# Kernel tuning notes

Measured on AMD Instinct MI355X. Metric: run time of the kernel, lower is better.

The kernel has to match this reference:

```python
import jax, jax.numpy as jnp
import numpy as np

N = 8192
F_IN = 512
F_OUT = 64
BETA = 0.5      # conf.beta
ALPHA = 0.2     # LeakyReLU negative slope
NEG_INF = -9e15


def setup_inputs() -> dict:
    key = jax.random.key(0)
    k1, k2, k3, k4, k5 = jax.random.split(key, 5)
    h = jax.random.normal(k1, (N, F_IN), dtype=jnp.float32)
    adj = jax.random.randint(k2, (N, N), 0, 2, dtype=jnp.int32)
    M = jax.random.uniform(k3, (N, N), dtype=jnp.float32)
    W = jax.random.normal(k4, (F_IN, F_OUT), dtype=jnp.float32) * (1.414 / np.sqrt(F_IN))
    a = jax.random.normal(k5, (2 * F_OUT, 1), dtype=jnp.float32) * 0.1
    return {"h": h, "adj": adj, "M": M, "W": W, "a": a}


def reference(h, adj, M, W, a):
    Wh = h @ W                                   # [N, F_OUT]
    adjf = adj.astype(Wh.dtype)
    H = BETA * M + (1.0 - BETA) * adjf           # [N, N] mixed adjacency
    # additive GAT score: e_ij = leakyrelu(a1.Wh_i + a2.(H Wh)_j)
    Wh1 = Wh @ a[:F_OUT]                         # [N, 1]
    Wh2 = (H @ Wh) @ a[F_OUT:]                   # [N, 1]
    e = jax.nn.leaky_relu(Wh1 + Wh2.T, negative_slope=ALPHA)  # [N, N]
    att = jnp.where(adj > 0, e, NEG_INF)
    att = jax.nn.softmax(att, axis=1)            # masked row softmax
    # dropout omitted (eval mode, training=False)
    h_prime = att @ Wh                           # [N, F_OUT]
    return jax.nn.elu(h_prime)                   # concat=True path
```

## Files before the change

### kernel.cpp

```cpp
#include <hip/hip_runtime.h>

#define NN 8192
#define FIN 512
#define FO 64

typedef __attribute__((ext_vector_type(8))) short short8;
typedef __attribute__((ext_vector_type(16))) float f32x16;
typedef __attribute__((ext_vector_type(4))) unsigned int uintx4;
typedef __attribute__((ext_vector_type(4))) int intv4;
typedef __attribute__((ext_vector_type(4))) float fltv4;
typedef unsigned short u16;
typedef unsigned int u32;
typedef unsigned long long u64;

__device__ inline u16 f2bf(float x) {
  u32 u = __builtin_bit_cast(u32, x);
  return (u16)((u + 0x7FFFu + ((u >> 16) & 1u)) >> 16);
}

__device__ inline u32 bfpack2(float a, float b, float& sum) {
  u32 ua = __builtin_bit_cast(u32, a);
  u32 ub = __builtin_bit_cast(u32, b);
  ua += 0x7FFFu + ((ua >> 16) & 1u);
  ub += 0x7FFFu + ((ub >> 16) & 1u);
  sum += __builtin_bit_cast(float, ua & 0xFFFF0000u);
  sum += __builtin_bit_cast(float, ub & 0xFFFF0000u);
  return (ua >> 16) | (ub & 0xFFFF0000u);
}

__global__ __launch_bounds__(256) void k1_wh(const float* __restrict__ h,
    const float* __restrict__ W, const float* __restrict__ a,
    float* __restrict__ s, float* __restrict__ v, u16* __restrict__ whb) {
  int tid = threadIdx.x;
  int row = blockIdx.x * 16 + (tid >> 4);
  int fq = (tid & 15) << 2;
  const float* hr = h + (size_t)row * FIN;
  float ax = 0.f, ay = 0.f, az = 0.f, aw = 0.f;
  #pragma unroll 4
  for (int k = 0; k < FIN; k += 4) {
    float4 h4 = *(const float4*)(hr + k);
    float4 w0 = *(const float4*)(W + (size_t)(k + 0) * FO + fq);
    float4 w1 = *(const float4*)(W + (size_t)(k + 1) * FO + fq);
    float4 w2 = *(const float4*)(W + (size_t)(k + 2) * FO + fq);
    float4 w3 = *(const float4*)(W + (size_t)(k + 3) * FO + fq);
    ax += h4.x * w0.x + h4.y * w1.x + h4.z * w2.x + h4.w * w3.x;
    ay += h4.x * w0.y + h4.y * w1.y + h4.z * w2.y + h4.w * w3.y;
    az += h4.x * w0.z + h4.y * w1.z + h4.z * w2.z + h4.w * w3.z;
    aw += h4.x * w0.w + h4.y * w1.w + h4.z * w2.w + h4.w * w3.w;
  }
  ushort4 st4;
  st4.x = f2bf(ax); st4.y = f2bf(ay); st4.z = f2bf(az); st4.w = f2bf(aw);
  *(ushort4*)(whb + (size_t)row * FO + fq) = st4;
  float4 a1 = *(const float4*)(a + fq);
  float4 a2 = *(const float4*)(a + FO + fq);
  float sp = ax * a1.x + ay * a1.y + az * a1.z + aw * a1.w;
  float vp = ax * a2.x + ay * a2.y + az * a2.z + aw * a2.w;
  #pragma unroll
  for (int d = 1; d < 16; d <<= 1) { sp += __shfl_xor(sp, d); vp += __shfl_xor(vp, d); }
  if ((tid & 15) == 0) { s[row] = sp; v[row] = vp; }
}

__global__ __launch_bounds__(256) void k1b_pack(const u16* __restrict__ whb,
                                               u16* __restrict__ bpack) {
  __shared__ __attribute__((aligned(16))) u16 ld[64 * 64];
  int tid = threadIdx.x;
  const uint4* src = (const uint4*)(whb + (size_t)blockIdx.x * 64 * 64);
  uint4* dst = (uint4*)ld;
  dst[tid] = src[tid];
  dst[tid + 256] = src[tid + 256];
  __syncthreads();
  int lane = tid & 63;
  int w = tid >> 6;
  int ks = blockIdx.x * 4 + w;
  int m = lane & 31;
  int half = lane >> 5;
  #pragma unroll
  for (int tt = 0; tt < 2; ++tt) {
    u32 o0, o1, o2, o3;
    int krow = w * 16 + half * 8;
    int n = tt * 32 + m;
    o0 = (u32)ld[(krow + 0) * 64 + n] | ((u32)ld[(krow + 1) * 64 + n] << 16);
    o1 = (u32)ld[(krow + 2) * 64 + n] | ((u32)ld[(krow + 3) * 64 + n] << 16);
    o2 = (u32)ld[(krow + 4) * 64 + n] | ((u32)ld[(krow + 5) * 64 + n] << 16);
    o3 = (u32)ld[(krow + 6) * 64 + n] | ((u32)ld[(krow + 7) * 64 + n] << 16);
    uint4 ov; ov.x = o0; ov.y = o1; ov.z = o2; ov.w = o3;
    *(uint4*)(bpack + (((size_t)ks * 2 + tt) * 64 + lane) * 8) = ov;
  }
}

__global__ __launch_bounds__(256) void k2_hv(const int* __restrict__ adj,
    const float* __restrict__ M, const float* __restrict__ v,
    float* __restrict__ t, u64* __restrict__ bm) {
  int i = blockIdx.x;
  int tid = threadIdx.x;
  int lane = tid & 63;
  int w = tid >> 6;
  const intv4* arow = (const intv4*)(adj + (size_t)i * NN);
  const fltv4* mrow = (const fltv4*)(M + (size_t)i * NN);
  const fltv4* v4 = (const fltv4*)v;
  float acc = 0.f;
  #pragma unroll
  for (int it = 0; it < 8; ++it) {
    int idx = it * 256 + tid;
    intv4 a4 = __builtin_nontemporal_load(arow + idx);
    fltv4 m4 = __builtin_nontemporal_load(mrow + idx);
    fltv4 vv = v4[idx];
    acc += m4.x * vv.x + m4.y * vv.y + m4.z * vv.z + m4.w * vv.w;
    acc += (a4.x ? vv.x : 0.f) + (a4.y ? vv.y : 0.f) + (a4.z ? vv.z : 0.f) + (a4.w ? vv.w : 0.f);
    u64 b0 = __ballot(a4.x != 0);
    u64 b1 = __ballot(a4.y != 0);
    u64 b2 = __ballot(a4.z != 0);
    u64 b3 = __ballot(a4.w != 0);
    if (lane == 0) {
      size_t base = (size_t)i * 128 + it * 16 + w * 4;
      bm[base + 0] = b0; bm[base + 1] = b1; bm[base + 2] = b2; bm[base + 3] = b3;
    }
  }
  #pragma unroll
  for (int d = 1; d < 64; d <<= 1) acc += __shfl_xor(acc, d);
  __shared__ float red[4];
  if (lane == 0) red[w] = acc;
  __syncthreads();
  if (tid == 0) t[i] = 0.5f * (red[0] + red[1] + red[2] + red[3]);
}

__device__ inline void stage_tile(const u16* __restrict__ bpack, u16* dstbase,
                                  int jt, int w, int lane) {
  const char* g0 = (const char*)bpack + (size_t)jt * 32768 + (size_t)lane * 16;
  #pragma unroll
  for (int cc = 0; cc < 8; ++cc) {
    int chunk = w * 8 + cc;
    const void* gp = g0 + chunk * 1024;
    void* lp = (char*)dstbase + chunk * 1024;
    __builtin_amdgcn_global_load_lds((const __attribute__((address_space(1))) u32*)gp,
                                     (__attribute__((address_space(3))) u32*)lp, 16, 0, 0);
  }
}

__global__ __launch_bounds__(256) void k3_att(const u16* __restrict__ bpack,
    const u64* __restrict__ bm, const float* __restrict__ t,
    const float* __restrict__ s, float* __restrict__ out) {
  __shared__ __attribute__((aligned(16))) u16 bbuf[2][16384];
  __shared__ __attribute__((aligned(16))) float accbuf[4 * 2 * 64 * 16];
  __shared__ float zbuf[4][64];
  __shared__ float wred[4];
  int tid = threadIdx.x;
  int lane = tid & 63;
  int w = tid >> 6;
  int m = lane & 31;
  int half = lane >> 5;
  int i0 = blockIdx.x << 5;
  int row = i0 + m;
  float srow = s[row];
  stage_tile(bpack, bbuf[0], 0, w, lane);
  float lmax = -3e38f;
  const float4* t4 = (const float4*)t;
  #pragma unroll
  for (int r = 0; r < 8; ++r) {
    float4 tv = t4[r * 256 + tid];
    lmax = fmaxf(fmaxf(lmax, fmaxf(tv.x, tv.y)), fmaxf(tv.z, tv.w));
  }
  #pragma unroll
  for (int d = 1; d < 64; d <<= 1) lmax = fmaxf(lmax, __shfl_xor(lmax, d));
  if (lane == 0) wred[w] = lmax;
  __syncthreads();
  float tmax = fmaxf(fmaxf(wred[0], wred[1]), fmaxf(wred[2], wred[3]));
  float um = srow + tmax;
  float mxv = fmaxf(um, 0.2f * um);

  f32x16 acc0, acc1;
  #pragma unroll
  for (int r = 0; r < 16; ++r) { acc0[r] = 0.f; acc1[r] = 0.f; }
  float zpart = 0.f;
  int cur = 0;
  for (int jt = 0; jt < 32; ++jt) {
    __syncthreads();
    if (jt + 1 < 32) stage_tile(bpack, bbuf[cur ^ 1], jt + 1, w, lane);
    const u64* wp = bm + (size_t)row * 128 + ((jt >> 2) << 4) + ((jt & 3) << 2);
    u64 wd0 = wp[0], wd1 = wp[1], wd2 = wp[2], wd3 = wp[3];
    const float* tb = t + (jt << 8) + (w << 6) + (half << 3);
    #pragma unroll
    for (int c = 0; c < 4; ++c) {
      int ks = (w << 2) + c;
      float4 t0 = *(const float4*)(tb + (c << 4));
      float4 t1 = *(const float4*)(tb + (c << 4) + 4);
      int sh = (w << 4) + (c << 2) + (half << 1);
      u32 q0 = (u32)(wd0 >> sh), q1 = (u32)(wd1 >> sh);
      u32 q2 = (u32)(wd2 >> sh), q3 = (u32)(wd3 >> sh);
      float u0 = srow + t0.x, u1 = srow + t0.y, u2 = srow + t0.z, u3 = srow + t0.w;
      float u4 = srow + t1.x, u5 = srow + t1.y, u6 = srow + t1.z, u7 = srow + t1.w;
      float g0 = __expf(fmaxf(u0, 0.2f * u0) - mxv);
      float g1 = __expf(fmaxf(u1, 0.2f * u1) - mxv);
      float g2 = __expf(fmaxf(u2, 0.2f * u2) - mxv);
      float g3 = __expf(fmaxf(u3, 0.2f * u3) - mxv);
      float g4 = __expf(fmaxf(u4, 0.2f * u4) - mxv);
      float g5 = __expf(fmaxf(u5, 0.2f * u5) - mxv);
      float g6 = __expf(fmaxf(u6, 0.2f * u6) - mxv);
      float g7 = __expf(fmaxf(u7, 0.2f * u7) - mxv);
      float w0 = (q0 & 1u) ? g0 : 0.f;
      float w1 = (q1 & 1u) ? g1 : 0.f;
      float w2 = (q2 & 1u) ? g2 : 0.f;
      float w3 = (q3 & 1u) ? g3 : 0.f;
      float w4 = (q0 & 2u) ? g4 : 0.f;
      float w5 = (q1 & 2u) ? g5 : 0.f;
      float w6 = (q2 & 2u) ? g6 : 0.f;
      float w7 = (q3 & 2u) ? g7 : 0.f;
      uintx4 awv;
      awv.x = bfpack2(w0, w1, zpart);
      awv.y = bfpack2(w2, w3, zpart);
      awv.z = bfpack2(w4, w5, zpart);
      awv.w = bfpack2(w6, w7, zpart);
      short8 af = __builtin_bit_cast(short8, awv);
      short8 b0 = *(const short8*)(bbuf[cur] + (((ks << 1) + 0) * 64 + lane) * 8);
      short8 b1 = *(const short8*)(bbuf[cur] + (((ks << 1) + 1) * 64 + lane) * 8);
      acc0 = __builtin_amdgcn_mfma_f32_32x32x16_bf16(af, b0, acc0, 0, 0, 0);
      acc1 = __builtin_amdgcn_mfma_f32_32x32x16_bf16(af, b1, acc1, 0, 0, 0);
    }
    cur ^= 1;
  }
  __syncthreads();
  zbuf[w][lane] = zpart;
  {
    float* ab = accbuf + (((w << 1) + 0) * 64 + lane) * 16;
    #pragma unroll
    for (int r = 0; r < 16; ++r) ab[r] = acc0[r];
    ab = accbuf + (((w << 1) + 1) * 64 + lane) * 16;
    #pragma unroll
    for (int r = 0; r < 16; ++r) ab[r] = acc1[r];
  }
  __syncthreads();
  int mm = tid >> 3;
  int fb = (tid & 7) << 3;
  float zr = 0.f;
  #pragma unroll
  for (int ww = 0; ww < 4; ++ww) zr += zbuf[ww][mm] + zbuf[ww][mm + 32];
  float inv = 1.f / zr;
  int reg = (mm & 3) + ((mm >> 3) << 2);
  int h2 = (mm >> 2) & 1;
  #pragma unroll
  for (int ff = 0; ff < 8; ++ff) {
    int f = fb + ff;
    int tt = f >> 5;
    int col = f & 31;
    float val = 0.f;
    #pragma unroll
    for (int ww = 0; ww < 4; ++ww)
      val += accbuf[(((ww << 1) + tt) * 64 + col + (h2 << 5)) * 16 + reg];
    float o = val * inv;
    out[((size_t)(i0 + mm) << 6) + f] = o > 0.f ? o : (__expf(o) - 1.f);
  }
}

extern "C" void kernel_launch(void* const* d_in, const int* in_sizes, int n_in,
                              void* d_out, int out_size, void* d_ws, size_t ws_size,
                              hipStream_t stream) {
  const float* h   = (const float*)d_in[0];
  const int*   adj = (const int*)d_in[1];
  const float* M   = (const float*)d_in[2];
  const float* W   = (const float*)d_in[3];
  const float* a   = (const float*)d_in[4];
  float* out = (float*)d_out;
  char* ws = (char*)d_ws;
  u64*  bm    = (u64*)ws;
  u16*  whb   = (u16*)(ws + (8u << 20));
  u16*  bpack = (u16*)(ws + (9u << 20));
  float* s    = (float*)(ws + (10u << 20));
  float* v    = (float*)(ws + (10u << 20) + 32768);
  float* t    = (float*)(ws + (10u << 20) + 65536);

  k1_wh  <<<512, 256, 0, stream>>>(h, W, a, s, v, whb);
  k1b_pack<<<128, 256, 0, stream>>>(whb, bpack);
  k2_hv  <<<NN, 256, 0, stream>>>(adj, M, v, t, bm);
  k3_att <<<256, 256, 0, stream>>>(bpack, bm, t, s, out);
}
```

Measured before the change: 598.2 us.

## Factor softmax exponentials into per-column tables and hoist the global max

The exponent exp(leakyrelu(s_i+t_j)-mx) is split into per-row constants times per-column factors exp(t_j-tmax) or exp(0.2(t_j-tmax)), chosen by the sign of s_i+t_j. A new single-block kernel computes tmax and the two column tables once, which removes per-element exp calls and the per-block max reduction from the attention kernel. In exchange it adds an extra launch and two more global loads per element, and the product form may overflow or underflow differently from the original.

```diff
diff --git a/kernel.cpp b/kernel.cpp
--- a/kernel.cpp
+++ b/kernel.cpp
@@ -124,6 +124,38 @@
   if (tid == 0) t[i] = 0.5f * (red[0] + red[1] + red[2] + red[3]);
 }
 
+__global__ __launch_bounds__(1024) void k2b_prep(const float* __restrict__ t,
+    float* __restrict__ f1, float* __restrict__ f2, float* __restrict__ tmaxg) {
+  __shared__ float red[16];
+  int tid = threadIdx.x;
+  const fltv4* t4 = (const fltv4*)t;
+  fltv4 a = t4[tid];
+  fltv4 b = t4[tid + 1024];
+  float lm = fmaxf(fmaxf(fmaxf(a.x, a.y), fmaxf(a.z, a.w)),
+                   fmaxf(fmaxf(b.x, b.y), fmaxf(b.z, b.w)));
+  #pragma unroll
+  for (int d = 1; d < 64; d <<= 1) lm = fmaxf(lm, __shfl_xor(lm, d));
+  if ((tid & 63) == 0) red[tid >> 6] = lm;
+  __syncthreads();
+  float tmax = red[0];
+  #pragma unroll
+  for (int r = 1; r < 16; ++r) tmax = fmaxf(tmax, red[r]);
+  if (tid == 0) tmaxg[0] = tmax;
+  fltv4 o;
+  o.x = __expf(a.x - tmax); o.y = __expf(a.y - tmax);
+  o.z = __expf(a.z - tmax); o.w = __expf(a.w - tmax);
+  ((fltv4*)f1)[tid] = o;
+  o.x = __expf(b.x - tmax); o.y = __expf(b.y - tmax);
+  o.z = __expf(b.z - tmax); o.w = __expf(b.w - tmax);
+  ((fltv4*)f1)[tid + 1024] = o;
+  o.x = __expf(0.2f * (a.x - tmax)); o.y = __expf(0.2f * (a.y - tmax));
+  o.z = __expf(0.2f * (a.z - tmax)); o.w = __expf(0.2f * (a.w - tmax));
+  ((fltv4*)f2)[tid] = o;
+  o.x = __expf(0.2f * (b.x - tmax)); o.y = __expf(0.2f * (b.y - tmax));
+  o.z = __expf(0.2f * (b.z - tmax)); o.w = __expf(0.2f * (b.w - tmax));
+  ((fltv4*)f2)[tid + 1024] = o;
+}
+
 __device__ inline void stage_tile(const u16* __restrict__ bpack, u16* dstbase,
                                   int jt, int w, int lane) {
   const char* g0 = (const char*)bpack + (size_t)jt * 32768 + (size_t)lane * 16;
@@ -139,11 +171,12 @@
 
 __global__ __launch_bounds__(256) void k3_att(const u16* __restrict__ bpack,
     const u64* __restrict__ bm, const float* __restrict__ t,
-    const float* __restrict__ s, float* __restrict__ out) {
+    const float* __restrict__ f1, const float* __restrict__ f2,
+    const float* __restrict__ s, const float* __restrict__ tmaxg,
+    float* __restrict__ out) {
   __shared__ __attribute__((aligned(16))) u16 bbuf[2][16384];
   __shared__ __attribute__((aligned(16))) float accbuf[4 * 2 * 64 * 16];
   __shared__ float zbuf[4][64];
-  __shared__ float wred[4];
   int tid = threadIdx.x;
   int lane = tid & 63;
   int w = tid >> 6;
@@ -151,22 +184,14 @@
   int half = lane >> 5;
   int i0 = blockIdx.x << 5;
   int row = i0 + m;
+  stage_tile(bpack, bbuf[0], 0, w, lane);
   float srow = s[row];
-  stage_tile(bpack, bbuf[0], 0, w, lane);
-  float lmax = -3e38f;
-  const float4* t4 = (const float4*)t;
-  #pragma unroll
-  for (int r = 0; r < 8; ++r) {
-    float4 tv = t4[r * 256 + tid];
-    lmax = fmaxf(fmaxf(lmax, fmaxf(tv.x, tv.y)), fmaxf(tv.z, tv.w));
-  }
-  #pragma unroll
-  for (int d = 1; d < 64; d <<= 1) lmax = fmaxf(lmax, __shfl_xor(lmax, d));
-  if (lane == 0) wred[w] = lmax;
-  __syncthreads();
-  float tmax = fmaxf(fmaxf(wred[0], wred[1]), fmaxf(wred[2], wred[3]));
+  float tmax = tmaxg[0];
   float um = srow + tmax;
   float mxv = fmaxf(um, 0.2f * um);
+  float E1 = __expf(um - mxv);
+  float E2 = __expf(0.2f * um - mxv);
+  float negs = -srow;
 
   f32x16 acc0, acc1;
   #pragma unroll
@@ -178,25 +203,30 @@
     if (jt + 1 < 32) stage_tile(bpack, bbuf[cur ^ 1], jt + 1, w, lane);
     const u64* wp = bm + (size_t)row * 128 + ((jt >> 2) << 4) + ((jt & 3) << 2);
     u64 wd0 = wp[0], wd1 = wp[1], wd2 = wp[2], wd3 = wp[3];
-    const float* tb = t + (jt << 8) + (w << 6) + (half << 3);
+    int off = (jt << 8) + (w << 6) + (half << 3);
+    const float* tb = t + off;
+    const float* p1 = f1 + off;
+    const float* p2 = f2 + off;
     #pragma unroll
     for (int c = 0; c < 4; ++c) {
       int ks = (w << 2) + c;
       float4 t0 = *(const float4*)(tb + (c << 4));
       float4 t1 = *(const float4*)(tb + (c << 4) + 4);
+      float4 A0 = *(const float4*)(p1 + (c << 4));
+      float4 A1 = *(const float4*)(p1 + (c << 4) + 4);
+      float4 B0 = *(const float4*)(p2 + (c << 4));
+      float4 B1 = *(const float4*)(p2 + (c << 4) + 4);
       int sh = (w << 4) + (c << 2) + (half << 1);
       u32 q0 = (u32)(wd0 >> sh), q1 = (u32)(wd1 >> sh);
       u32 q2 = (u32)(wd2 >> sh), q3 = (u32)(wd3 >> sh);
-      float u0 = srow + t0.x, u1 = srow + t0.y, u2 = srow + t0.z, u3 = srow + t0.w;
-      float u4 = srow + t1.x, u5 = srow + t1.y, u6 = srow + t1.z, u7 = srow + t1.w;
-      float g0 = __expf(fmaxf(u0, 0.2f * u0) - mxv);
-      float g1 = __expf(fmaxf(u1, 0.2f * u1) - mxv);
-      float g2 = __expf(fmaxf(u2, 0.2f * u2) - mxv);
-      float g3 = __expf(fmaxf(u3, 0.2f * u3) - mxv);
-      float g4 = __expf(fmaxf(u4, 0.2f * u4) - mxv);
-      float g5 = __expf(fmaxf(u5, 0.2f * u5) - mxv);
-      float g6 = __expf(fmaxf(u6, 0.2f * u6) - mxv);
-      float g7 = __expf(fmaxf(u7, 0.2f * u7) - mxv);
+      float g0 = (t0.x >= negs) ? E1 * A0.x : E2 * B0.x;
+      float g1 = (t0.y >= negs) ? E1 * A0.y : E2 * B0.y;
+      float g2 = (t0.z >= negs) ? E1 * A0.z : E2 * B0.z;
+      float g3 = (t0.w >= negs) ? E1 * A0.w : E2 * B0.w;
+      float g4 = (t1.x >= negs) ? E1 * A1.x : E2 * B1.x;
+      float g5 = (t1.y >= negs) ? E1 * A1.y : E2 * B1.y;
+      float g6 = (t1.z >= negs) ? E1 * A1.z : E2 * B1.z;
+      float g7 = (t1.w >= negs) ? E1 * A1.w : E2 * B1.w;
       float w0 = (q0 & 1u) ? g0 : 0.f;
       float w1 = (q1 & 1u) ? g1 : 0.f;
       float w2 = (q2 & 1u) ? g2 : 0.f;
@@ -267,9 +297,13 @@
   float* s    = (float*)(ws + (10u << 20));
   float* v    = (float*)(ws + (10u << 20) + 32768);
   float* t    = (float*)(ws + (10u << 20) + 65536);
-
-  k1_wh  <<<512, 256, 0, stream>>>(h, W, a, s, v, whb);
+  float* f1   = (float*)(ws + (10u << 20) + 98304);
+  float* f2   = (float*)(ws + (10u << 20) + 131072);
+  float* tmx  = (float*)(ws + (10u << 20) + 163840);
+
+  k1_wh   <<<512, 256, 0, stream>>>(h, W, a, s, v, whb);
   k1b_pack<<<128, 256, 0, stream>>>(whb, bpack);
-  k2_hv  <<<NN, 256, 0, stream>>>(adj, M, v, t, bm);
-  k3_att <<<256, 256, 0, stream>>>(bpack, bm, t, s, out);
-}
+  k2_hv   <<<NN, 256, 0, stream>>>(adj, M, v, t, bm);
+  k2b_prep<<<1, 1024, 0, stream>>>(t, f1, f2, tmx);
+  k3_att  <<<256, 256, 0, stream>>>(bpack, bm, t, f1, f2, s, tmx, out);
+}
```

Result: slower. 615.6 us (+2.9%).
